# Kernel tuning notes

Hardware: AMD Instinct MI355X
Metric: run time of the kernel (lower is better)

The kernel has to match this reference:

```python
import jax, jax.numpy as jnp
import numpy as np

B, M = 4, 8192
NUM_PAD = 1024  # trailing pc columns zeroed to exercise the zero-column mask


def setup_inputs() -> dict:
    key = jax.random.key(0)
    k1, k2 = jax.random.split(key)
    vertices = jax.random.normal(k1, (B, 3, 128, 64), dtype=jnp.float32)
    pc = jax.random.normal(k2, (B, 3, M), dtype=jnp.float32)
    # zero-pad some columns: the original filters columns where all 3 coords == 0
    pc = pc.at[:, :, M - NUM_PAD:].set(0.0)
    return {"vertices": vertices, "pc": pc}


def reference(vertices, pc):
    b = vertices.shape[0]
    v = vertices.reshape(b, 3, -1).transpose(0, 2, 1)   # [B, N, 3] mesh vertices
    p = pc.transpose(0, 2, 1)                           # [B, M, 3] point cloud
    valid = ~jnp.all(pc == 0.0, axis=1)                 # [B, M] non-zero columns
    # squared pairwise distances pc -> vertices: [B, M, N]
    d2 = (
        jnp.sum(p * p, axis=-1)[:, :, None]
        + jnp.sum(v * v, axis=-1)[:, None, :]
        - 2.0 * jnp.einsum("bmd,bnd->bmn", p, v)
    )
    dist2 = jnp.min(d2, axis=-1)                        # [B, M] NN sq-dist per pc point
    valid_f = valid.astype(dist2.dtype)
    per_item = jnp.sum(dist2 * valid_f, axis=-1) / jnp.sum(valid_f, axis=-1)  # mean over valid points
    return jnp.mean(per_item)
```

## Files before the change

kernel.cpp:

```cpp
#include <hip/hip_runtime.h>

typedef float v2f __attribute__((ext_vector_type(2)));

#define MPTS 8192
#define NVERT 8192
#define TPB 256
#define PPT 4
#define BQ (TPB*PPT)
#define VC 512

static __device__ __forceinline__ unsigned int enc_f32(float f) {
    unsigned int b = __float_as_uint(f);
    return (b & 0x80000000u) ? ~b : (b | 0x80000000u);
}
static __device__ __forceinline__ float dec_f32(unsigned int e) {
    unsigned int b = (e & 0x80000000u) ? (e & 0x7FFFFFFFu) : ~e;
    return __uint_as_float(b);
}

__global__ __launch_bounds__(TPB) void minpart_kernel(
        const float* __restrict__ vert,
        const float* __restrict__ pc,
        unsigned int* __restrict__ wsmin)
{
    __shared__ float4 lvA[VC / 2];
    __shared__ float4 lvB[VC / 2];
    const int b = blockIdx.z, vbase = blockIdx.y * VC, mbase = blockIdx.x * BQ;
    const int tid = threadIdx.x;

    const float* pcb = pc + (size_t)b * 3 * MPTS;
    v2f npx[PPT], npy[PPT], npz[PPT];
    int mm[PPT];
    #pragma unroll
    for (int p = 0; p < PPT; ++p) {
        const int m = mbase + tid + p * TPB;
        mm[p] = m;
        const float x = pcb[m], y = pcb[MPTS + m], z = pcb[2 * MPTS + m];
        npx[p] = (v2f){-2.0f * x, -2.0f * x};
        npy[p] = (v2f){-2.0f * y, -2.0f * y};
        npz[p] = (v2f){-2.0f * z, -2.0f * z};
    }

    const float* vb = vert + (size_t)b * 3 * NVERT + vbase;
    const v2f* vbx = (const v2f*)(vb);
    const v2f* vby = (const v2f*)(vb + NVERT);
    const v2f* vbz = (const v2f*)(vb + 2 * NVERT);
    for (int i = tid; i < VC / 2; i += TPB) {
        const v2f x = vbx[i], y = vby[i], z = vbz[i];
        const v2f w = x * x + y * y + z * z;
        lvA[i] = make_float4(x.x, x.y, y.x, y.y);
        lvB[i] = make_float4(z.x, z.y, w.x, w.y);
    }
    __syncthreads();

    v2f acc[PPT];
    #pragma unroll
    for (int p = 0; p < PPT; ++p) acc[p] = (v2f){1e30f, 1e30f};

    #pragma unroll 4
    for (int j = 0; j < VC / 2; ++j) {
        const float4 A = lvA[j], Bv = lvB[j];
        const v2f vx = {A.x, A.y}, vy = {A.z, A.w};
        const v2f vz = {Bv.x, Bv.y}, vw = {Bv.z, Bv.w};
        #pragma unroll
        for (int p = 0; p < PPT; ++p) {
            const v2f t = __builtin_elementwise_fma(npx[p], vx,
                           __builtin_elementwise_fma(npy[p], vy,
                            __builtin_elementwise_fma(npz[p], vz, vw)));
            acc[p] = __builtin_elementwise_min(acc[p], t);
        }
    }

    unsigned int* wm = wsmin + (size_t)b * MPTS;
    #pragma unroll
    for (int p = 0; p < PPT; ++p)
        atomicMin(&wm[mm[p]], enc_f32(fminf(acc[p].x, acc[p].y)));
}

__global__ __launch_bounds__(256) void reduce_kernel(
        const float* __restrict__ pc,
        const unsigned int* __restrict__ wsmin,
        v2f* __restrict__ part)
{
    const int b = blockIdx.x >> 3, sl = blockIdx.x & 7;
    const int tid = threadIdx.x;
    const float* pcb = pc + (size_t)b * 3 * MPTS;
    const unsigned int* wm = wsmin + (size_t)b * MPTS;

    float sum = 0.0f, cnt = 0.0f;
    #pragma unroll
    for (int k = 0; k < 4; ++k) {
        const int m = sl * 1024 + k * 256 + tid;
        const float x = pcb[m], y = pcb[MPTS + m], z = pcb[2 * MPTS + m];
        const float t = dec_f32(wm[m]);
        const float d2 = fmaf(x, x, fmaf(y, y, fmaf(z, z, t)));
        if (!(x == 0.0f && y == 0.0f && z == 0.0f)) { sum += d2; cnt += 1.0f; }
    }
    for (int off = 32; off; off >>= 1) {
        sum += __shfl_down(sum, off);
        cnt += __shfl_down(cnt, off);
    }
    __shared__ float ss[4], sc[4];
    const int wid = tid >> 6, lane = tid & 63;
    if (lane == 0) { ss[wid] = sum; sc[wid] = cnt; }
    __syncthreads();
    if (tid == 0)
        part[blockIdx.x] = (v2f){ss[0] + ss[1] + ss[2] + ss[3],
                                 sc[0] + sc[1] + sc[2] + sc[3]};
}

__global__ __launch_bounds__(64) void final_kernel(
        const v2f* __restrict__ part, float* __restrict__ out, int B)
{
    const int lane = threadIdx.x;
    float s = 0.0f, c = 0.0f;
    if (lane < B * 8) { const v2f p = part[lane]; s = p.x; c = p.y; }
    #pragma unroll
    for (int off = 4; off; off >>= 1) {
        s += __shfl_down(s, off);
        c += __shfl_down(c, off);
    }
    const float r = s / c;
    float acc = 0.0f;
    for (int g = 0; g < B; ++g) acc += __shfl(r, g * 8);
    if (lane == 0) out[0] = acc / (float)B;
}

extern "C" void kernel_launch(void* const* d_in, const int* in_sizes, int n_in,
                              void* d_out, int out_size, void* d_ws, size_t ws_size,
                              hipStream_t stream) {
    const float* vert = (const float*)d_in[0];
    const float* pc   = (const float*)d_in[1];
    float* out        = (float*)d_out;
    const int B = in_sizes[0] / (3 * NVERT);

    unsigned int* wsmin = (unsigned int*)d_ws;
    v2f* part = (v2f*)(wsmin + (size_t)B * MPTS);
    hipMemsetAsync(wsmin, 0xFF, (size_t)B * MPTS * sizeof(unsigned int), stream);

    dim3 grid(MPTS / BQ, NVERT / VC, B);
    minpart_kernel<<<grid, TPB, 0, stream>>>(vert, pc, wsmin);
    reduce_kernel<<<B * 8, 256, 0, stream>>>(pc, wsmin, part);
    final_kernel<<<1, 64, 0, stream>>>(part, out, B);
}
```

Measured before the change: 78.30 us.

## Replace atomicMin with per-chunk partial minima and drop LDS vertex staging

```diff
diff --git a/kernel.cpp b/kernel.cpp
--- a/kernel.cpp
+++ b/kernel.cpp
@@ -5,53 +5,35 @@
 #define MPTS 8192
 #define NVERT 8192
 #define TPB 256
-#define PPT 4
+#define PPT 8
 #define BQ (TPB*PPT)
-#define VC 512
-
-static __device__ __forceinline__ unsigned int enc_f32(float f) {
-    unsigned int b = __float_as_uint(f);
-    return (b & 0x80000000u) ? ~b : (b | 0x80000000u);
-}
-static __device__ __forceinline__ float dec_f32(unsigned int e) {
-    unsigned int b = (e & 0x80000000u) ? (e & 0x7FFFFFFFu) : ~e;
-    return __uint_as_float(b);
-}
+#define NCHUNK 32
+#define VC (NVERT/NCHUNK)
 
 __global__ __launch_bounds__(TPB) void minpart_kernel(
         const float* __restrict__ vert,
         const float* __restrict__ pc,
-        unsigned int* __restrict__ wsmin)
+        float* __restrict__ partial)
 {
-    __shared__ float4 lvA[VC / 2];
-    __shared__ float4 lvB[VC / 2];
-    const int b = blockIdx.z, vbase = blockIdx.y * VC, mbase = blockIdx.x * BQ;
+    const int b = blockIdx.z, chunk = blockIdx.y;
+    const int mbase = blockIdx.x * BQ;
     const int tid = threadIdx.x;
 
     const float* pcb = pc + (size_t)b * 3 * MPTS;
     v2f npx[PPT], npy[PPT], npz[PPT];
-    int mm[PPT];
     #pragma unroll
     for (int p = 0; p < PPT; ++p) {
-        const int m = mbase + tid + p * TPB;
-        mm[p] = m;
+        const int m = mbase + p * TPB + tid;
         const float x = pcb[m], y = pcb[MPTS + m], z = pcb[2 * MPTS + m];
         npx[p] = (v2f){-2.0f * x, -2.0f * x};
         npy[p] = (v2f){-2.0f * y, -2.0f * y};
         npz[p] = (v2f){-2.0f * z, -2.0f * z};
     }
 
-    const float* vb = vert + (size_t)b * 3 * NVERT + vbase;
+    const float* vb = vert + (size_t)b * 3 * NVERT + chunk * VC;
     const v2f* vbx = (const v2f*)(vb);
     const v2f* vby = (const v2f*)(vb + NVERT);
     const v2f* vbz = (const v2f*)(vb + 2 * NVERT);
-    for (int i = tid; i < VC / 2; i += TPB) {
-        const v2f x = vbx[i], y = vby[i], z = vbz[i];
-        const v2f w = x * x + y * y + z * z;
-        lvA[i] = make_float4(x.x, x.y, y.x, y.y);
-        lvB[i] = make_float4(z.x, z.y, w.x, w.y);
-    }
-    __syncthreads();
 
     v2f acc[PPT];
     #pragma unroll
@@ -59,9 +41,8 @@
 
     #pragma unroll 4
     for (int j = 0; j < VC / 2; ++j) {
-        const float4 A = lvA[j], Bv = lvB[j];
-        const v2f vx = {A.x, A.y}, vy = {A.z, A.w};
-        const v2f vz = {Bv.x, Bv.y}, vw = {Bv.z, Bv.w};
+        const v2f vx = vbx[j], vy = vby[j], vz = vbz[j];
+        const v2f vw = vx * vx + vy * vy + vz * vz;
         #pragma unroll
         for (int p = 0; p < PPT; ++p) {
             const v2f t = __builtin_elementwise_fma(npx[p], vx,
@@ -71,28 +52,31 @@
         }
     }
 
-    unsigned int* wm = wsmin + (size_t)b * MPTS;
+    float* po = partial + ((size_t)b * NCHUNK + chunk) * MPTS + mbase + tid;
     #pragma unroll
     for (int p = 0; p < PPT; ++p)
-        atomicMin(&wm[mm[p]], enc_f32(fminf(acc[p].x, acc[p].y)));
+        po[p * TPB] = fminf(acc[p].x, acc[p].y);
 }
 
 __global__ __launch_bounds__(256) void reduce_kernel(
         const float* __restrict__ pc,
-        const unsigned int* __restrict__ wsmin,
+        const float* __restrict__ partial,
         v2f* __restrict__ part)
 {
     const int b = blockIdx.x >> 3, sl = blockIdx.x & 7;
     const int tid = threadIdx.x;
     const float* pcb = pc + (size_t)b * 3 * MPTS;
-    const unsigned int* wm = wsmin + (size_t)b * MPTS;
+    const float* pb  = partial + (size_t)b * NCHUNK * MPTS;
 
     float sum = 0.0f, cnt = 0.0f;
     #pragma unroll
     for (int k = 0; k < 4; ++k) {
         const int m = sl * 1024 + k * 256 + tid;
+        float t = pb[m];
+        #pragma unroll
+        for (int c = 1; c < NCHUNK; ++c)
+            t = fminf(t, pb[(size_t)c * MPTS + m]);
         const float x = pcb[m], y = pcb[MPTS + m], z = pcb[2 * MPTS + m];
-        const float t = dec_f32(wm[m]);
         const float d2 = fmaf(x, x, fmaf(y, y, fmaf(z, z, t)));
         if (!(x == 0.0f && y == 0.0f && z == 0.0f)) { sum += d2; cnt += 1.0f; }
     }
@@ -134,12 +118,11 @@
     float* out        = (float*)d_out;
     const int B = in_sizes[0] / (3 * NVERT);
 
-    unsigned int* wsmin = (unsigned int*)d_ws;
-    v2f* part = (v2f*)(wsmin + (size_t)B * MPTS);
-    hipMemsetAsync(wsmin, 0xFF, (size_t)B * MPTS * sizeof(unsigned int), stream);
+    float* partial = (float*)d_ws;
+    v2f* part = (v2f*)(partial + (size_t)B * NCHUNK * MPTS);
 
-    dim3 grid(MPTS / BQ, NVERT / VC, B);
-    minpart_kernel<<<grid, TPB, 0, stream>>>(vert, pc, wsmin);
-    reduce_kernel<<<B * 8, 256, 0, stream>>>(pc, wsmin, part);
+    dim3 grid(MPTS / BQ, NCHUNK, B);
+    minpart_kernel<<<grid, TPB, 0, stream>>>(vert, pc, partial);
+    reduce_kernel<<<B * 8, 256, 0, stream>>>(pc, partial, part);
     final_kernel<<<1, 64, 0, stream>>>(part, out, B);
 }
```

Measured after the change: 83.06 us. 1.06x slower.
